# Performance work log

Hardware: AMD Instinct MI355X
Metric: run time of the kernel (lower is better)

Reference implementation:

```python
import jax, jax.numpy as jnp
import numpy as np

DECAY = 0.4  # from x_f + 0.6*y_{f-1} + 3 - y_{f-1} == x_f - 0.4*y_{f-1} + 3
BIAS = 3.0


def setup_inputs() -> dict:
    key = jax.random.key(0)
    x = jax.random.normal(key, (8, 16, 3, 224, 224), dtype=jnp.float32)
    return {"x": x}


def reference(x) -> jnp.ndarray:
    # Faithful translation of Temporal.forward, including the aliasing /
    # repeated-zeroing semantics of rgb_differ (traced from the source):
    #   - batch 0:   y[0]=x[0];  y[f] = x[f] - 0.4*y[f-1] + 3   (data recurrence)
    #   - batches 1..b-2: all zeros (re-zeroed by each later outer iteration)
    #   - batch b-1: z[0]=0;     z[f] = 3 - 0.4*z[f-1]          (scalar recurrence,
    #                 broadcast over c,h,w; input-independent)
    # then permute(0,1,4,3,2): [b,t,c,h,w] -> [b,t,w,h,c].
    b, t = x.shape[0], x.shape[1]

    # batch-0 data-dependent recurrence over time via scan (elementwise in c,h,w)
    def step(carry, xt):
        y = xt - DECAY * carry + BIAS
        return y, y

    y0_first = x[0, 0]                                   # [c,h,w]
    _, y0_rest = jax.lax.scan(step, y0_first, x[0, 1:])  # [t-1,c,h,w]
    y0 = jnp.concatenate([y0_first[None], y0_rest], axis=0)  # [t,c,h,w]

    out = jnp.zeros_like(x).at[0].set(y0)

    if b > 1:
        # last-batch input-independent scalar recurrence, broadcast spatially
        def zstep(c, _):
            z = BIAS - DECAY * c
            return z, z

        _, z_rest = jax.lax.scan(zstep, jnp.float32(0.0), None, length=t - 1)
        z = jnp.concatenate([jnp.zeros((1,), x.dtype), z_rest.astype(x.dtype)])  # [t]
        out = out.at[-1].set(jnp.broadcast_to(z[:, None, None, None], x.shape[1:]))

    return jnp.transpose(out, (0, 1, 4, 3, 2))  # [b,t,w,h,c]
```

## Files before the change

### kernel.cpp

```cpp
#include <hip/hip_runtime.h>


typedef float fx4 __attribute__((ext_vector_type(4)));

#define SP        150528
#define TT        16
#define CH_STRIDE 50176
#define BSTRIDE   2408448

#define NWT    7
#define NTILES 196

#define FILL4   4214784
#define TSLICE4 37632
#define NBLOCKS 2048
#define NFILL   (NBLOCKS - NTILES)
#define RFILL   2276
#define SPREAD  9

__global__ __launch_bounds__(256) void temporal_fused(
    const float* __restrict__ x, float* __restrict__ out)
{
    const int tid = threadIdx.x;
    const int bid = blockIdx.x;

    __shared__ float lds[4 * 768];

    const bool is_tile = (bid % SPREAD == 0) && (bid / SPREAD) < NTILES;

    if (is_tile) {
        const int tileid = bid / SPREAD;
        const int h0 = (tileid / NWT) * 8;
        const int w0 = (tileid % NWT) * 32;
        const int dw = tid & 31;
        const int hh = tid >> 5;
        const int rbase = (h0 + hh) * 224 + w0 + dw;

        float v[TT][3];
        #pragma unroll
        for (int t = 0; t < TT; ++t) {
            #pragma unroll
            for (int c = 0; c < 3; ++c)
                v[t][c] = x[t * SP + c * CH_STRIDE + rbase];
        }

        int wbase[3];
        #pragma unroll
        for (int c = 0; c < 3; ++c) {
            const int idx = hh * 3 + c;
            const int s = idx >> 2, o = idx & 3;
            wbase[c] = dw * 24 + ((s + dw) % 6) * 4 + o;
        }

        const int ob0 = w0 * 672 + h0 * 3;
        float y0 = 0.f, y1 = 0.f, y2 = 0.f;

        #pragma unroll
        for (int p = 0; p < 4; ++p) {
            #pragma unroll
            for (int tl = 0; tl < 4; ++tl) {
                const int t = p * 4 + tl;
                if (t == 0) { y0 = v[0][0]; y1 = v[0][1]; y2 = v[0][2]; }
                else {
                    y0 = v[t][0] - 0.4f * y0 + 3.0f;
                    y1 = v[t][1] - 0.4f * y1 + 3.0f;
                    y2 = v[t][2] - 0.4f * y2 + 3.0f;
                }
                lds[tl * 768 + wbase[0]] = y0;
                lds[tl * 768 + wbase[1]] = y1;
                lds[tl * 768 + wbase[2]] = y2;
            }
            __syncthreads();

            const fx4* lds4 = reinterpret_cast<const fx4*>(lds);
            #pragma unroll
            for (int k = 0; k < 3; ++k) {
                const int j = tid + k * 256;
                const int tl = j / 192;
                const int r = j - tl * 192;
                const int w = r / 6;
                const int piece = r - w * 6;
                const int phys = (piece + w) % 6;
                const fx4 f4 = lds4[(tl * 768 + w * 24 + phys * 4) >> 2];
                *reinterpret_cast<fx4*>(
                    out + (p * 4 + tl) * SP + ob0 + w * 672 + piece * 4) = f4;
            }
            __syncthreads();
        }
        return;
    }

    const int tiles_before = min((bid + SPREAD - 1) / SPREAD, NTILES);
    const int fidx = bid - tiles_before;

    fx4* out4 = reinterpret_cast<fx4*>(out + BSTRIDE);
    int q   = fidx * RFILL;
    int end = q + RFILL;
    if (end > FILL4) end = FILL4;

    while (q < end) {
        const int slice = q / TSLICE4;
        int send = (slice + 1) * TSLICE4;
        if (send > end) send = end;
        float zv = 0.0f;
        if ((slice >> 4) == 6) {
            const int t = slice & 15;
            float z = 0.0f;
            for (int i = 0; i < t; ++i) z = 3.0f - 0.4f * z;
            zv = z;
        }
        fx4 val;
        val.x = zv; val.y = zv; val.z = zv; val.w = zv;
        for (int i = q + tid; i < send; i += 256)
            out4[i] = val;
        q = send;
    }
}

extern "C" void kernel_launch(void* const* d_in, const int* in_sizes, int n_in,
                              void* d_out, int out_size, void* d_ws, size_t ws_size,
                              hipStream_t stream) {
    const float* x = (const float*)d_in[0];
    float* out = (float*)d_out;
    temporal_fused<<<NBLOCKS, 256, 0, stream>>>(x, out);
}
```

Baseline: 17.30 us.

## Use larger 32x32 spatial tiles with double-buffered time-pair loads

Each batch-0 tile block now covers a 32x32 spatial tile with 4 rows per thread, giving 49 tile blocks instead of 196. Input loads are software-pipelined two timesteps ahead, and each output write covers 96 contiguous floats per w instead of 24. The goal is longer contiguous transposed stores and hiding load latency behind compute. The cost is fewer, heavier tile blocks with higher register pressure, which may make them the critical path while the fill blocks finish sooner.

```diff
diff --git a/kernel.cpp b/kernel.cpp
--- a/kernel.cpp
+++ b/kernel.cpp
@@ -8,15 +8,15 @@
 #define CH_STRIDE 50176
 #define BSTRIDE   2408448
 
-#define NWT    7
-#define NTILES 196
+#define NWT2   7
+#define NTILES 49
+#define TSPREAD 41
 
 #define FILL4   4214784
 #define TSLICE4 37632
 #define NBLOCKS 2048
 #define NFILL   (NBLOCKS - NTILES)
-#define RFILL   2276
-#define SPREAD  9
+#define RFILL   2109
 
 __global__ __launch_bounds__(256) void temporal_fused(
     const float* __restrict__ x, float* __restrict__ out)
@@ -24,73 +24,100 @@
     const int tid = threadIdx.x;
     const int bid = blockIdx.x;
 
-    __shared__ float lds[4 * 768];
+    __shared__ float lds[2 * 32 * 96];
 
-    const bool is_tile = (bid % SPREAD == 0) && (bid / SPREAD) < NTILES;
+    const bool is_tile = (bid % TSPREAD == 0) && (bid / TSPREAD) < NTILES;
 
     if (is_tile) {
-        const int tileid = bid / SPREAD;
-        const int h0 = (tileid / NWT) * 8;
-        const int w0 = (tileid % NWT) * 32;
+        const int tileid = bid / TSPREAD;
+        const int h0 = (tileid / NWT2) * 32;
+        const int w0 = (tileid % NWT2) * 32;
         const int dw = tid & 31;
-        const int hh = tid >> 5;
-        const int rbase = (h0 + hh) * 224 + w0 + dw;
+        const int hq = tid >> 5;
 
-        float v[TT][3];
+        int rbase[4];
         #pragma unroll
-        for (int t = 0; t < TT; ++t) {
+        for (int i = 0; i < 4; ++i)
+            rbase[i] = (h0 + hq * 4 + i) * 224 + w0 + dw;
+
+        int woff[4][3];
+        #pragma unroll
+        for (int i = 0; i < 4; ++i) {
             #pragma unroll
-            for (int c = 0; c < 3; ++c)
-                v[t][c] = x[t * SP + c * CH_STRIDE + rbase];
+            for (int c = 0; c < 3; ++c) {
+                const int idx = (hq * 4 + i) * 3 + c;
+                const int s = idx >> 2, o = idx & 3;
+                woff[i][c] = dw * 96 + ((s + dw) % 24) * 4 + o;
+            }
         }
 
-        int wbase[3];
+        float y[4][3];
+        float xc[2][4][3], xn[2][4][3];
         #pragma unroll
-        for (int c = 0; c < 3; ++c) {
-            const int idx = hh * 3 + c;
-            const int s = idx >> 2, o = idx & 3;
-            wbase[c] = dw * 24 + ((s + dw) % 6) * 4 + o;
-        }
+        for (int tp = 0; tp < 2; ++tp)
+            #pragma unroll
+            for (int i = 0; i < 4; ++i)
+                #pragma unroll
+                for (int c = 0; c < 3; ++c)
+                    xc[tp][i][c] = x[tp * SP + c * CH_STRIDE + rbase[i]];
 
         const int ob0 = w0 * 672 + h0 * 3;
-        float y0 = 0.f, y1 = 0.f, y2 = 0.f;
 
         #pragma unroll
-        for (int p = 0; p < 4; ++p) {
+        for (int p = 0; p < 8; ++p) {
+            if (p < 7) {
+                #pragma unroll
+                for (int tp = 0; tp < 2; ++tp)
+                    #pragma unroll
+                    for (int i = 0; i < 4; ++i)
+                        #pragma unroll
+                        for (int c = 0; c < 3; ++c)
+                            xn[tp][i][c] =
+                                x[((p + 1) * 2 + tp) * SP + c * CH_STRIDE + rbase[i]];
+            }
             #pragma unroll
-            for (int tl = 0; tl < 4; ++tl) {
-                const int t = p * 4 + tl;
-                if (t == 0) { y0 = v[0][0]; y1 = v[0][1]; y2 = v[0][2]; }
-                else {
-                    y0 = v[t][0] - 0.4f * y0 + 3.0f;
-                    y1 = v[t][1] - 0.4f * y1 + 3.0f;
-                    y2 = v[t][2] - 0.4f * y2 + 3.0f;
+            for (int tp = 0; tp < 2; ++tp) {
+                const int t = p * 2 + tp;
+                #pragma unroll
+                for (int i = 0; i < 4; ++i) {
+                    #pragma unroll
+                    for (int c = 0; c < 3; ++c) {
+                        const float xv = xc[tp][i][c];
+                        y[i][c] = (t == 0) ? xv : (xv - 0.4f * y[i][c] + 3.0f);
+                        lds[tp * 3072 + woff[i][c]] = y[i][c];
+                    }
                 }
-                lds[tl * 768 + wbase[0]] = y0;
-                lds[tl * 768 + wbase[1]] = y1;
-                lds[tl * 768 + wbase[2]] = y2;
             }
             __syncthreads();
 
             const fx4* lds4 = reinterpret_cast<const fx4*>(lds);
             #pragma unroll
-            for (int k = 0; k < 3; ++k) {
+            for (int k = 0; k < 6; ++k) {
                 const int j = tid + k * 256;
-                const int tl = j / 192;
-                const int r = j - tl * 192;
-                const int w = r / 6;
-                const int piece = r - w * 6;
-                const int phys = (piece + w) % 6;
-                const fx4 f4 = lds4[(tl * 768 + w * 24 + phys * 4) >> 2];
+                const int tp = j >> 9 >> 0 ? (j / 768) : 0;
+                const int jt = j / 768;
+                const int r = j - jt * 768;
+                const int w = r / 24;
+                const int piece = r - w * 24;
+                const int phys = (piece + w) % 24;
+                const fx4 f4 = lds4[jt * 768 + w * 24 + phys];
                 *reinterpret_cast<fx4*>(
-                    out + (p * 4 + tl) * SP + ob0 + w * 672 + piece * 4) = f4;
+                    out + (p * 2 + jt) * SP + ob0 + w * 672 + piece * 4) = f4;
             }
             __syncthreads();
+
+            #pragma unroll
+            for (int tp = 0; tp < 2; ++tp)
+                #pragma unroll
+                for (int i = 0; i < 4; ++i)
+                    #pragma unroll
+                    for (int c = 0; c < 3; ++c)
+                        xc[tp][i][c] = xn[tp][i][c];
         }
         return;
     }
 
-    const int tiles_before = min((bid + SPREAD - 1) / SPREAD, NTILES);
+    const int tiles_before = min((bid + TSPREAD - 1) / TSPREAD, NTILES);
     const int fidx = bid - tiles_before;
 
     fx4* out4 = reinterpret_cast<fx4*>(out + BSTRIDE);
```

Result: slower. 22.01 us (+27.2%).
